# Performance work log

Measured on AMD Instinct MI355X. Metric: run time of the kernel, lower is better.

## Reference

```python
import jax, jax.numpy as jnp
import numpy as np

N_USERS = 1024
N_ITEMS = 2048
N = N_USERS + N_ITEMS          # 3072 total nodes
D = 128                        # latent_dim_rec
L = 3                          # n_layers
K = [64, 64, 64]               # top-k per layer for getMaskAdj
GAMMA = 0.2                    # residual weight on svd embeddings
X_SCALE = 1.0                  # delta
B = 8192                       # batch of (user, item) pairs


def setup_inputs() -> dict:
    key = jax.random.key(0)
    ks = jax.random.split(key, 9)
    # normalized-adjacency-like dense graph: nonnegative, row sums ~ 1
    A = jax.random.uniform(ks[0], (N, N), dtype=jnp.float32) * (2.0 / N)
    user_emb = jax.random.normal(ks[1], (N_USERS, D), dtype=jnp.float32)
    item_emb = jax.random.normal(ks[2], (N_ITEMS, D), dtype=jnp.float32)
    user_emb0 = jax.random.normal(ks[3], (N_USERS, D), dtype=jnp.float32)
    item_emb0 = jax.random.normal(ks[4], (N_ITEMS, D), dtype=jnp.float32)
    vector_u = jax.random.uniform(ks[5], (1, N), dtype=jnp.float32)
    vector_v = jax.random.uniform(ks[6], (1, N), dtype=jnp.float32)
    users = jax.random.randint(ks[7], (B,), 0, N_USERS)
    items = jax.random.randint(ks[8], (B,), 0, N_ITEMS)
    return {
        "users": users, "items": items, "A": A,
        "user_emb": user_emb, "item_emb": item_emb,
        "user_emb0": user_emb0, "item_emb0": item_emb0,
        "vector_u": vector_u, "vector_v": vector_v,
    }


def topk_mask(M, k):
    """Keep top-k entries per row of M, zero elsewhere (getMaskAdj)."""
    vals, idx = jax.lax.top_k(M, k)          # [N,k], [N,k]
    rows = jnp.arange(M.shape[0])[:, None]
    return jnp.zeros_like(M).at[rows, idx].set(vals)


def _computer(A, user_emb, item_emb, user_emb0, item_emb0, vector_u, vector_v):
    all_emb = jnp.concatenate([user_emb, item_emb], axis=0)      # [N,D]
    all_emb0 = jnp.concatenate([user_emb0, item_emb0], axis=0)   # [N,D]
    u = vector_u[0]  # [N]
    v = vector_v[0]  # [N]

    # ---- computAttention: w_k = u A^k v for k = 0..L (A^0 = I via A_0=eye) ----
    w_list = [jnp.dot(u, v)]
    powers = []           # A^1 .. A^L (g_droped progression)
    Ak = A
    for layer in range(L):
        powers.append(Ak)
        w_list.append(jnp.dot(u, Ak @ v))
        if layer < L - 1:
            Ak = A @ Ak   # g_droped = Graph @ A_k
    w = jnp.stack(w_list)                 # [L+1]
    w = w / jnp.sum(w)
    attention_weight = jax.nn.softmax(w)  # softmax(dim=0)

    # ---- getMaskAdj: top-k masked powers ----
    A_list = [topk_mask(powers[l], K[l]) if K[l] != 0 else powers[l] for l in range(L)]

    # ---- layer-wise propagation with attention-weighted accumulation ----
    emb0 = all_emb
    light_out = X_SCALE * attention_weight[0] * all_emb
    for layer in range(L):
        e = A_list[layer] @ emb0 + GAMMA * all_emb0   # SpMM + residual
        light_out = light_out + X_SCALE * attention_weight[layer + 1] * e
    users_all = light_out[:N_USERS]
    items_all = light_out[N_USERS:]
    return users_all, items_all


def reference(users, items, A, user_emb, item_emb, user_emb0, item_emb0, vector_u, vector_v):
    users_all, items_all = _computer(A, user_emb, item_emb, user_emb0, item_emb0, vector_u, vector_v)
    u_e = users_all[users]   # [B,D]
    i_e = items_all[items]   # [B,D]
    return jnp.sum(u_e * i_e, axis=1)  # [B]
```

## Files before the change

kernel.cpp:

```cpp
#include <hip/hip_runtime.h>
#include <hip/hip_fp8.h>
#include <math.h>

#define NN 3072
#define NU 1024
#define NI 2048
#define DD 128
#define BB 8192
#define GAMMA_F 0.2f

#define SCALE_A 524288.0f
#define F8SCALE2 1.9073486328125e-06f
#define DESCALE38 3.637978807091713e-12f

#define KBLK ((size_t)NN * 64)

typedef __attribute__((ext_vector_type(4))) float f32x4;
typedef __attribute__((ext_vector_type(16))) float f32x16;
typedef __attribute__((ext_vector_type(4))) int i32x4;
typedef __attribute__((ext_vector_type(8))) int i32x8;

static __device__ inline unsigned short bf16bits(float x) {
  union { unsigned u; float f; } cv;
  cv.f = x;
  unsigned r = cv.u + 0x7fff + ((cv.u >> 16) & 1);
  return (unsigned short)(r >> 16);
}

static __device__ inline unsigned pk4_f8(float a, float b, float c, float d) {
#if defined(__has_builtin)
#if __has_builtin(__builtin_amdgcn_cvt_pk_fp8_f32)
  int p = __builtin_amdgcn_cvt_pk_fp8_f32(a, b, 0, false);
  p = __builtin_amdgcn_cvt_pk_fp8_f32(c, d, p, true);
  return (unsigned)p;
#else
  return (unsigned)__hip_fp8_e4m3(a).__x | ((unsigned)__hip_fp8_e4m3(b).__x << 8) |
         ((unsigned)__hip_fp8_e4m3(c).__x << 16) |
         ((unsigned)__hip_fp8_e4m3(d).__x << 24);
#endif
#else
  return (unsigned)__hip_fp8_e4m3(a).__x | ((unsigned)__hip_fp8_e4m3(b).__x << 8) |
         ((unsigned)__hip_fp8_e4m3(c).__x << 16) |
         ((unsigned)__hip_fp8_e4m3(d).__x << 24);
#endif
}

static __device__ inline void atomAddF(float* p, float v) {
#if defined(__has_builtin)
#if __has_builtin(__builtin_amdgcn_global_atomic_fadd_f32)
  __builtin_amdgcn_global_atomic_fadd_f32(
      (__attribute__((address_space(1))) float*)p, v);
#else
  unsafeAtomicAdd(p, v);
#endif
#else
  unsafeAtomicAdd(p, v);
#endif
}

static __device__ inline float block_sum(float s, float* red4) {
  int tid = threadIdx.x;
  for (int off = 32; off; off >>= 1) s += __shfl_down(s, off, 64);
  if ((tid & 63) == 0) red4[tid >> 6] = s;
  __syncthreads();
  return red4[0] + red4[1] + red4[2] + red4[3];
}

static __device__ inline float row_dot_f32(const float* __restrict__ a,
                                           const float* __restrict__ b,
                                           float* red4) {
  const float4* ap = (const float4*)a;
  const float4* bp = (const float4*)b;
  float s = 0.f;
  for (int j = threadIdx.x; j < NN / 4; j += 256) {
    float4 x = ap[j], y = bp[j];
    s += x.x * y.x + x.y * y.y + x.z * y.z + x.w * y.w;
  }
  return block_sum(s, red4);
}

static __device__ inline void load48_bf(const unsigned short* __restrict__ b0,
                                        int parts, int row, int lane,
                                        float* f) {
  const uint4* r0 = (const uint4*)(b0 + (size_t)row * NN);
#pragma unroll
  for (int j = 0; j < 6; ++j) {
    uint4 q = r0[lane + j * 64];
    unsigned uu[4] = {q.x, q.y, q.z, q.w};
#pragma unroll
    for (int e = 0; e < 4; ++e) {
      f[j * 8 + e * 2] = __uint_as_float(uu[e] << 16);
      f[j * 8 + e * 2 + 1] = __uint_as_float(uu[e] & 0xffff0000u);
    }
  }
  for (int p = 1; p < parts; ++p) {
    const uint4* rp = (const uint4*)(b0 + (size_t)p * NN * NN + (size_t)row * NN);
#pragma unroll
    for (int j = 0; j < 6; ++j) {
      uint4 q = rp[lane + j * 64];
      unsigned uu[4] = {q.x, q.y, q.z, q.w};
#pragma unroll
      for (int e = 0; e < 4; ++e) {
        f[j * 8 + e * 2] += __uint_as_float(uu[e] << 16);
        f[j * 8 + e * 2 + 1] += __uint_as_float(uu[e] & 0xffff0000u);
      }
    }
  }
}

static __device__ inline void load48_f32(const float* __restrict__ A, int row,
                                         int lane, float* f) {
  const float4* r0 = (const float4*)(A + (size_t)row * NN);
#pragma unroll
  for (int j = 0; j < 12; ++j) {
    float4 a = r0[lane + j * 64];
    f[j * 4 + 0] = a.x; f[j * 4 + 1] = a.y;
    f[j * 4 + 2] = a.z; f[j * 4 + 3] = a.w;
  }
}

static __device__ void select_compact(const float* f, int lane, float descale,
                                      int bf, int* __restrict__ outCnt,
                                      int* __restrict__ outIdx,
                                      float* __restrict__ outVal) {
  unsigned bor = 0, band = 0xffffffffu;
#pragma unroll
  for (int r = 0; r < 48; ++r) {
    unsigned k = __float_as_uint(f[r]);
    bor |= k; band &= k;
  }
  for (int off = 32; off; off >>= 1) {
    bor |= (unsigned)__shfl_xor((int)bor, off, 64);
    band &= (unsigned)__shfl_xor((int)band, off, 64);
  }
  unsigned diff = bor ^ band;
  int hi = diff ? (31 - __clz(diff)) : 16;
  if (hi < 16) hi = 16;
  if (hi > 30) hi = 30;
  unsigned t = band & ~((2u << hi) - 1u);

  int b = hi;
  while (b >= 17) {
    unsigned base = 1u << (b - 1);
    unsigned cand1 = t | base;
    unsigned cand2 = t | (base << 1);
    unsigned cand3 = cand2 | base;
    int c1 = 0, c2 = 0, c3 = 0;
#pragma unroll
    for (int r = 0; r < 48; ++r) {
      unsigned k = __float_as_uint(f[r]);
      c1 += (k >= cand1) ? 1 : 0;
      c2 += (k >= cand2) ? 1 : 0;
      c3 += (k >= cand3) ? 1 : 0;
    }
    for (int off = 32; off; off >>= 1) {
      c1 += __shfl_xor(c1, off, 64);
      c2 += __shfl_xor(c2, off, 64);
      c3 += __shfl_xor(c3, off, 64);
    }
    if (c3 >= 64) t = cand3;
    else if (c2 >= 64) t = cand2;
    else if (c1 >= 64) t = cand1;
    b -= 2;
  }
  if (b == 16) {
    unsigned cand = t | (1u << 16);
    int c = 0;
#pragma unroll
    for (int r = 0; r < 48; ++r) c += (__float_as_uint(f[r]) >= cand) ? 1 : 0;
    for (int off = 32; off; off >>= 1) c += __shfl_xor(c, off, 64);
    if (c >= 64) t = cand;
  }

  int basec = 0;
#pragma unroll
  for (int r = 0; r < 48; ++r) {
    bool keep = __float_as_uint(f[r]) >= t;
    unsigned long long m = __ballot(keep);
    if (keep) {
      int pos = basec + __popcll(m & ((1ull << lane) - 1ull));
      if (pos < 128) {
        int col = bf ? ((r >> 3) * 512 + lane * 8 + (r & 7))
                     : ((r >> 2) * 256 + lane * 4 + (r & 3));
        outIdx[pos] = col << 7;
        outVal[pos] = f[r] * descale;
      }
    }
    basec += __popcll(m);
  }
  if (lane == 0) *outCnt = basec < 128 ? basec : 128;
}

__global__ __launch_bounds__(256) void prep(
    const float* __restrict__ A, const float* __restrict__ vu,
    const float* __restrict__ vv, unsigned char* __restrict__ Af8,
    unsigned char* __restrict__ Atf8, float* __restrict__ y1,
    float* __restrict__ s1) {
  __shared__ float sh[64 * 65 + 512];
  const int bid = blockIdx.x;
  const int t = threadIdx.x;
  const int bx = (bid % 48) * 64, by = (bid / 48) * 64;
  const int rr = t >> 4;
  const int c4 = (t & 15) * 4;
  for (int it = 0; it < 4; ++it) {
    int r = rr + it * 16;
    float4 val = *(const float4*)(A + (size_t)(by + r) * NN + bx + c4);
    sh[r * 65 + c4] = val.x; sh[r * 65 + c4 + 1] = val.y;
    sh[r * 65 + c4 + 2] = val.z; sh[r * 65 + c4 + 3] = val.w;
  }
  __syncthreads();
  {
    int row = t >> 2, ch = t & 3;
    const float* sp = &sh[row * 65 + ch * 16];
    uint4 w;
    w.x = pk4_f8(sp[0] * SCALE_A, sp[1] * SCALE_A, sp[2] * SCALE_A,
                 sp[3] * SCALE_A);
    w.y = pk4_f8(sp[4] * SCALE_A, sp[5] * SCALE_A, sp[6] * SCALE_A,
                 sp[7] * SCALE_A);
    w.z = pk4_f8(sp[8] * SCALE_A, sp[9] * SCALE_A, sp[10] * SCALE_A,
                 sp[11] * SCALE_A);
    w.w = pk4_f8(sp[12] * SCALE_A, sp[13] * SCALE_A, sp[14] * SCALE_A,
                 sp[15] * SCALE_A);
    *(uint4*)(Af8 + (size_t)(bx >> 6) * KBLK + (size_t)(by + row) * 64 +
              ch * 16) = w;
  }
  {
    int c = t >> 2, ch = t & 3;
    float v[16];
#pragma unroll
    for (int e = 0; e < 16; ++e) v[e] = sh[(ch * 16 + e) * 65 + c];
    uint4 w;
    w.x = pk4_f8(v[0] * SCALE_A, v[1] * SCALE_A, v[2] * SCALE_A,
                 v[3] * SCALE_A);
    w.y = pk4_f8(v[4] * SCALE_A, v[5] * SCALE_A, v[6] * SCALE_A,
                 v[7] * SCALE_A);
    w.z = pk4_f8(v[8] * SCALE_A, v[9] * SCALE_A, v[10] * SCALE_A,
                 v[11] * SCALE_A);
    w.w = pk4_f8(v[12] * SCALE_A, v[13] * SCALE_A, v[14] * SCALE_A,
                 v[15] * SCALE_A);
    *(uint4*)(Atf8 + (size_t)(by >> 6) * KBLK + (size_t)(bx + c) * 64 +
              ch * 16) = w;
  }
  const int q = t >> 6;
  const int l = t & 63;
  float sy = 0.f, ss_ = 0.f;
  for (int i = 0; i < 16; ++i) {
    int c = q * 16 + i;
    sy += sh[l * 65 + c] * vv[bx + c];
    ss_ += vu[by + c] * sh[c * 65 + l];
  }
  float* red = sh + 64 * 65;
  red[q * 64 + l] = sy;
  red[256 + q * 64 + l] = ss_;
  __syncthreads();
  if (t < 64) {
    float v4 = red[t] + red[64 + t] + red[128 + t] + red[192 + t];
    atomAddF(&y1[by + t], v4);
  } else if (t < 128) {
    int cc = t - 64;
    float v4 = red[256 + cc] + red[256 + 64 + cc] + red[256 + 128 + cc] +
               red[256 + 192 + cc];
    atomAddF(&s1[bx + cc], v4);
  }
}

#define MFMA4(A0, A1, B0, B1)                                          \
  acc[0][0] = __builtin_amdgcn_mfma_scale_f32_32x32x64_f8f6f4(         \
      A0, B0, acc[0][0], 0, 0, 0, 127, 0, 127);                        \
  acc[0][1] = __builtin_amdgcn_mfma_scale_f32_32x32x64_f8f6f4(         \
      A0, B1, acc[0][1], 0, 0, 0, 127, 0, 127);                        \
  acc[1][0] = __builtin_amdgcn_mfma_scale_f32_32x32x64_f8f6f4(         \
      A1, B0, acc[1][0], 0, 0, 0, 127, 0, 127);                        \
  acc[1][1] = __builtin_amdgcn_mfma_scale_f32_32x32x64_f8f6f4(         \
      A1, B1, acc[1][1], 0, 0, 0, 127, 0, 127);

static __device__ inline i32x8 ldfragL(const char* p) {
  i32x4 lo = *(const i32x4*)p;
  i32x4 hi = *(const i32x4*)(p + 1024);
  return (i32x8){lo.x, lo.y, lo.z, lo.w, hi.x, hi.y, hi.z, hi.w};
}

__global__ __launch_bounds__(256) void gemm_f8(
    const unsigned char* __restrict__ Ag,
    const unsigned char* __restrict__ Btg,
    unsigned short* __restrict__ Cg) {
  __shared__ char smem[2][16384];
  const int wg = blockIdx.x;
  const int xcd = wg & 7;
  const int idx = wg >> 3;
  const int bxi = xcd * 3 + (idx % 3);
  const int byi = idx / 3;
  const int rowBase = byi * 128, colBase = bxi * 128;

  const int t = threadIdx.x;
  const int w = t >> 6, l = t & 63;
  const int wr = w >> 1, wc = w & 1;
  const int r32 = l & 31, hh = l >> 5;

  f32x16 acc[2][2];
  for (int i = 0; i < 2; ++i)
    for (int j = 0; j < 2; ++j)
      for (int e = 0; e < 16; ++e) acc[i][j][e] = 0.f;

  const unsigned char* aT = Ag + (size_t)rowBase * 64;
  const unsigned char* bT = Btg + (size_t)colBase * 64;
  const int laneOff = r32 * 64 + hh * 32;

#define STAGE(kt, b)                                                        \
  {                                                                         \
    const size_t kOff = (size_t)(kt) * KBLK;                                \
    _Pragma("unroll") for (int r_ = 0; r_ < 4; ++r_) {                      \
      int q_ = r_ * 4 + w;                                                  \
      int s_ = (q_ >> 1) & 3, h_ = q_ & 1;                                  \
      const unsigned char* g_ = ((q_ < 8) ? aT : bT) + kOff +               \
                                (size_t)(s_ * 32) * 64 + laneOff + h_ * 16; \
      __builtin_amdgcn_global_load_lds(                                     \
          (const __attribute__((address_space(1))) unsigned*)g_,            \
          (__attribute__((address_space(3))) unsigned*)(smem[b] +           \
                                                        q_ * 1024),         \
          16, 0, 0);                                                        \
    }                                                                       \
  }

  const int nt = NN / 64;
  STAGE(0, 0);
  __syncthreads();
  int cur = 0;
  for (int kt = 0; kt < nt; ++kt) {
    if (kt + 1 < nt) STAGE(kt + 1, cur ^ 1);
    const char* sb = smem[cur];
    i32x8 a0 = ldfragL(sb + (wr * 2 + 0) * 2048 + l * 16);
    i32x8 a1 = ldfragL(sb + (wr * 2 + 1) * 2048 + l * 16);
    i32x8 b0 = ldfragL(sb + 8192 + (wc * 2 + 0) * 2048 + l * 16);
    i32x8 b1 = ldfragL(sb + 8192 + (wc * 2 + 1) * 2048 + l * 16);
    MFMA4(a0, a1, b0, b1);
    __syncthreads();
    cur ^= 1;
  }
#undef STAGE

  for (int i = 0; i < 2; ++i) {
    int rb = rowBase + wr * 64 + i * 32 + 4 * hh;
    for (int j = 0; j < 2; ++j) {
      int cc = colBase + wc * 64 + j * 32 + r32;
      for (int reg = 0; reg < 16; ++reg) {
        int rr = rb + (reg & 3) + 8 * (reg >> 2);
        Cg[(size_t)rr * NN + cc] = bf16bits(acc[i][j][reg]);
      }
    }
  }
}

__global__ __launch_bounds__(256) void post1(
    const unsigned short* __restrict__ C, int parts,
    const float* __restrict__ A, const float* __restrict__ y1,
    unsigned char* __restrict__ A2f8, int* __restrict__ cnts1,
    int* __restrict__ tIdx1, float* __restrict__ tVal1,
    float* __restrict__ tvec, const float* __restrict__ uemb,
    const float* __restrict__ iemb, float* __restrict__ allE) {
  const int bid = blockIdx.x;
  const int t = threadIdx.x;
  if (bid < 768) {
    int row = bid * 4 + (t >> 6);
    int lane = t & 63;
    float f[48];
    load48_bf(C, parts, row, lane, f);
#pragma unroll
    for (int j = 0; j < 6; ++j) {
      uint2 w;
      w.x = pk4_f8(f[j * 8 + 0] * F8SCALE2, f[j * 8 + 1] * F8SCALE2,
                   f[j * 8 + 2] * F8SCALE2, f[j * 8 + 3] * F8SCALE2);
      w.y = pk4_f8(f[j * 8 + 4] * F8SCALE2, f[j * 8 + 5] * F8SCALE2,
                   f[j * 8 + 6] * F8SCALE2, f[j * 8 + 7] * F8SCALE2);
      size_t addr = (size_t)(j * 8 + (lane >> 3)) * KBLK +
                    (size_t)row * 64 + (lane & 7) * 8;
      *(uint2*)(A2f8 + addr) = w;
    }
    select_compact(f, lane, DESCALE38, 1, &cnts1[row],
                   tIdx1 + (size_t)row * 128, tVal1 + (size_t)row * 128);
  } else if (bid < 1536) {
    int row = (bid - 768) * 4 + (t >> 6);
    int lane = t & 63;
    const float4* rp = (const float4*)(A + (size_t)row * NN);
    const float4* yp = (const float4*)y1;
    float s = 0.f;
#pragma unroll
    for (int j = 0; j < 12; ++j) {
      float4 a = rp[lane + j * 64];
      float4 y = yp[lane + j * 64];
      s += a.x * y.x + a.y * y.y + a.z * y.z + a.w * y.w;
    }
    for (int off = 32; off; off >>= 1) s += __shfl_down(s, off, 64);
    if (lane == 0) tvec[row] = s;
  } else {
    int idx = (bid - 1536) * 256 + t;
    int e = idx * 4;
    float4 v = (e < NU * DD) ? *(const float4*)(uemb + e)
                             : *(const float4*)(iemb + (e - NU * DD));
    *(float4*)(allE + e) = v;
  }
}

__global__ __launch_bounds__(256) void post2(
    const float* __restrict__ vu, const float* __restrict__ vv,
    const float* __restrict__ y1, const float* __restrict__ s1,
    const float* __restrict__ tvec, float* __restrict__ wacc) {
  __shared__ float red4[4];
  const int t = threadIdx.x;
  float w0 = row_dot_f32(vu, vv, red4);  __syncthreads();
  float w1 = row_dot_f32(vu, y1, red4);  __syncthreads();
  float w2 = row_dot_f32(s1, y1, red4);  __syncthreads();
  float w3 = row_dot_f32(s1, tvec, red4);
  if (t == 0) { wacc[0] = w0; wacc[1] = w1; wacc[2] = w2; wacc[3] = w3; }
}

__global__ __launch_bounds__(256) void sel02(
    const unsigned short* __restrict__ C, int parts,
    const float* __restrict__ A, int* __restrict__ cnt0,
    int* __restrict__ idx0, float* __restrict__ val0,
    int* __restrict__ cnt2, int* __restrict__ idx2,
    float* __restrict__ val2) {
  const int bid = blockIdx.x;
  const int t = threadIdx.x;
  const int w = t >> 6, lane = t & 63;
  const int row = (bid >> 1) * 4 + w;
  float f[48];
  if ((bid & 1) == 0) {
    load48_bf(C, parts, row, lane, f);
    select_compact(f, lane, DESCALE38, 1, &cnt2[row],
                   idx2 + (size_t)row * 128, val2 + (size_t)row * 128);
  } else {
    load48_f32(A, row, lane, f);
    select_compact(f, lane, 1.0f, 0, &cnt0[row],
                   idx0 + (size_t)row * 128, val0 + (size_t)row * 128);
  }
}

__global__ __launch_bounds__(256) void gather_light(
    const float* __restrict__ allE, const float* __restrict__ uemb0,
    const float* __restrict__ iemb0, const float* __restrict__ wacc,
    const int* __restrict__ cnt0, const int* __restrict__ idx0,
    const float* __restrict__ val0, const int* __restrict__ cnts1,
    const int* __restrict__ tIdx1, const float* __restrict__ tVal1,
    const int* __restrict__ cnt2, const int* __restrict__ idx2,
    const float* __restrict__ val2, float* __restrict__ lightOut) {
  __shared__ int li[4][384];
  __shared__ float lv[4][384];
  const int t = threadIdx.x;
  const int w = t >> 6, lane = t & 63;
  const int row = blockIdx.x * 4 + w;

  float w0 = wacc[0], w1 = wacc[1], w2 = wacc[2], w3 = wacc[3];
  float ss = w0 + w1 + w2 + w3;
  w0 /= ss; w1 /= ss; w2 /= ss; w3 /= ss;
  float m = fmaxf(fmaxf(w0, w1), fmaxf(w2, w3));
  float ex0 = expf(w0 - m), ex1 = expf(w1 - m), ex2 = expf(w2 - m),
        ex3 = expf(w3 - m);
  float se = ex0 + ex1 + ex2 + ex3;
  float aw0 = ex0 / se, aw1 = ex1 / se, aw2 = ex2 / se, aw3 = ex3 / se;
  float aw4 = GAMMA_F * (aw1 + aw2 + aw3);

  const int c0 = cnt0[row], c1 = cnts1[row], c2 = cnt2[row];
  const int p0 = (c0 + 7) & ~7, p1 = (c1 + 7) & ~7, p2 = (c2 + 7) & ~7;
  int* Li = li[w];
  float* Lv = lv[w];
  const size_t rb = (size_t)row * 128;
  for (int k = lane; k < p0; k += 64) {
    bool in = k < c0;
    Li[k] = in ? idx0[rb + k] : 0;
    Lv[k] = in ? aw1 * val0[rb + k] : 0.f;
  }
  for (int k = lane; k < p1; k += 64) {
    bool in = k < c1;
    Li[p0 + k] = in ? tIdx1[rb + k] : 0;
    Lv[p0 + k] = in ? aw2 * tVal1[rb + k] : 0.f;
  }
  for (int k = lane; k < p2; k += 64) {
    bool in = k < c2;
    Li[p0 + p1 + k] = in ? idx2[rb + k] : 0;
    Lv[p0 + p1 + k] = in ? aw3 * val2[rb + k] : 0.f;
  }

  const int ct = p0 + p1 + p2;
  const float2* E2 = (const float2*)allE;
  float ax = 0.f, ay = 0.f, bx_ = 0.f, by_ = 0.f;
  for (int k = 0; k < ct; k += 8) {
    int i0 = Li[k + 0], i1 = Li[k + 1], i2 = Li[k + 2], i3 = Li[k + 3];
    int i4 = Li[k + 4], i5 = Li[k + 5], i6 = Li[k + 6], i7 = Li[k + 7];
    float v0 = Lv[k + 0], v1 = Lv[k + 1], v2 = Lv[k + 2], v3 = Lv[k + 3];
    float v4 = Lv[k + 4], v5 = Lv[k + 5], v6 = Lv[k + 6], v7 = Lv[k + 7];
    float2 g0 = E2[(i0 >> 1) + lane];
    float2 g1 = E2[(i1 >> 1) + lane];
    float2 g2 = E2[(i2 >> 1) + lane];
    float2 g3 = E2[(i3 >> 1) + lane];
    float2 g4 = E2[(i4 >> 1) + lane];
    float2 g5 = E2[(i5 >> 1) + lane];
    float2 g6 = E2[(i6 >> 1) + lane];
    float2 g7 = E2[(i7 >> 1) + lane];
    ax += v0 * g0.x; ay += v0 * g0.y;
    bx_ += v1 * g1.x; by_ += v1 * g1.y;
    ax += v2 * g2.x; ay += v2 * g2.y;
    bx_ += v3 * g3.x; by_ += v3 * g3.y;
    ax += v4 * g4.x; ay += v4 * g4.y;
    bx_ += v5 * g5.x; by_ += v5 * g5.y;
    ax += v6 * g6.x; ay += v6 * g6.y;
    bx_ += v7 * g7.x; by_ += v7 * g7.y;
  }
  float2 sE = E2[((size_t)row << 6) + lane];
  float2 e0 = (row < NU)
                  ? ((const float2*)uemb0)[(size_t)row * 64 + lane]
                  : ((const float2*)iemb0)[(size_t)(row - NU) * 64 + lane];
  float ox = (ax + bx_) + aw0 * sE.x + aw4 * e0.x;
  float oy = (ay + by_) + aw0 * sE.y + aw4 * e0.y;
  float2 o; o.x = ox; o.y = oy;
  ((float2*)lightOut)[(size_t)row * 64 + lane] = o;
}

__global__ __launch_bounds__(256) void out_dot(const int* __restrict__ users,
                                               const int* __restrict__ items,
                                               const float* __restrict__ lightOut,
                                               float* __restrict__ out) {
  int b = blockIdx.x * 4 + (threadIdx.x >> 6);
  int lane = threadIdx.x & 63;
  const float* up = lightOut + (size_t)users[b] * DD;
  const float* ip = lightOut + (size_t)(NU + items[b]) * DD;
  float s = up[lane] * ip[lane] + up[lane + 64] * ip[lane + 64];
  for (int off = 32; off; off >>= 1) s += __shfl_down(s, off, 64);
  if (lane == 0) out[b] = s;
}

extern "C" void kernel_launch(void* const* d_in, const int* in_sizes, int n_in,
                              void* d_out, int out_size, void* d_ws,
                              size_t ws_size, hipStream_t stream) {
  const int* users = (const int*)d_in[0];
  const int* items = (const int*)d_in[1];
  const float* A = (const float*)d_in[2];
  const float* uemb = (const float*)d_in[3];
  const float* iemb = (const float*)d_in[4];
  const float* uemb0 = (const float*)d_in[5];
  const float* iemb0 = (const float*)d_in[6];
  const float* vu = (const float*)d_in[7];
  const float* vv = (const float*)d_in[8];
  float* out = (float*)d_out;

  char* ws = (char*)d_ws;
  size_t off = 0;
  auto alloc = [&](size_t bytes) -> void* {
    void* p = ws + off;
    off += (bytes + 255) & ~(size_t)255;
    return p;
  };
  unsigned char* Af8 = (unsigned char*)alloc((size_t)NN * NN);
  unsigned char* Atf8 = (unsigned char*)alloc((size_t)NN * NN);
  unsigned char* A2f8 = (unsigned char*)alloc((size_t)NN * NN);
  float* y1 = (float*)alloc((size_t)NN * 4);
  float* s1 = (float*)alloc((size_t)NN * 4);
  float* tvec = (float*)alloc((size_t)NN * 4);
  float* wacc = (float*)alloc(256);
  int* cnts1 = (int*)alloc((size_t)NN * 4);
  int* tIdx1 = (int*)alloc((size_t)NN * 128 * 4);
  float* tVal1 = (float*)alloc((size_t)NN * 128 * 4);
  float* lightOut = (float*)alloc((size_t)NN * DD * 4);
  int* cnt0 = (int*)alloc((size_t)NN * 4);
  int* cnt2 = (int*)alloc((size_t)NN * 4);

  float* allE = (float*)Af8;
  const size_t LSTB = (size_t)NN * 128 * 4;
  int* idx0 = (int*)(Atf8);
  float* val0 = (float*)(Atf8 + LSTB);
  int* idx2 = (int*)(Atf8 + 2 * LSTB);
  float* val2 = (float*)(Atf8 + 3 * LSTB);

  unsigned short* C = (unsigned short*)alloc((size_t)NN * NN * 2);

  hipMemsetAsync(y1, 0, (size_t)2 * NN * 4, stream);
  prep<<<2304, 256, 0, stream>>>(A, vu, vv, Af8, Atf8, y1, s1);
  gemm_f8<<<576, 256, 0, stream>>>(Af8, Atf8, C);
  post1<<<1920, 256, 0, stream>>>(C, 1, A, y1, A2f8, cnts1, tIdx1,
                                  tVal1, tvec, uemb, iemb, allE);
  gemm_f8<<<576, 256, 0, stream>>>(A2f8, Atf8, C);
  sel02<<<1536, 256, 0, stream>>>(C, 1, A, cnt0, idx0, val0, cnt2, idx2,
                                  val2);
  post2<<<1, 256, 0, stream>>>(vu, vv, y1, s1, tvec, wacc);
  gather_light<<<768, 256, 0, stream>>>(allE, uemb0, iemb0, wacc, cnt0, idx0,
                                        val0, cnts1, tIdx1, tVal1, cnt2, idx2,
                                        val2, lightOut);
  out_dot<<<BB / 4, 256, 0, stream>>>(users, items, lightOut, out);
}
```

Baseline: 263.9 us.

## Triple-buffer FP8 GEMM pipeline and fold small kernels into neighbors

The FP8 GEMM moves from a double-buffered LDS pipeline to a triple-buffered one. It prefetches two K-tiles ahead, waits on explicit vmcnt instead of full syncthreads, and raises wave priority around the MFMAs. The embedding concat copy moves from post1 into extra prep blocks, writing to a dedicated allE buffer instead of aliasing Af8. The single-block attention-weight reduction kernel is merged into sel02 as one extra block, which removes a launch. The triple buffer uses more LDS per block, and the relaxed barrier protocol relies on the vmcnt counts being correct.

```diff
diff --git a/kernel.cpp b/kernel.cpp
--- a/kernel.cpp
+++ b/kernel.cpp
@@ -195,10 +195,19 @@
     const float* __restrict__ A, const float* __restrict__ vu,
     const float* __restrict__ vv, unsigned char* __restrict__ Af8,
     unsigned char* __restrict__ Atf8, float* __restrict__ y1,
-    float* __restrict__ s1) {
+    float* __restrict__ s1, const float* __restrict__ uemb,
+    const float* __restrict__ iemb, float* __restrict__ allE) {
   __shared__ float sh[64 * 65 + 512];
   const int bid = blockIdx.x;
   const int t = threadIdx.x;
+  if (bid >= 2304) {
+    int idx = (bid - 2304) * 256 + t;
+    int e = idx * 4;
+    float4 v = (e < NU * DD) ? *(const float4*)(uemb + e)
+                             : *(const float4*)(iemb + (e - NU * DD));
+    *(float4*)(allE + e) = v;
+    return;
+  }
   const int bx = (bid % 48) * 64, by = (bid / 48) * 64;
   const int rr = t >> 4;
   const int c4 = (t & 15) * 4;
@@ -284,7 +293,7 @@
     const unsigned char* __restrict__ Ag,
     const unsigned char* __restrict__ Btg,
     unsigned short* __restrict__ Cg) {
-  __shared__ char smem[2][16384];
+  __shared__ char smem[3][16384];
   const int wg = blockIdx.x;
   const int xcd = wg & 7;
   const int idx = wg >> 3;
@@ -324,18 +333,25 @@
 
   const int nt = NN / 64;
   STAGE(0, 0);
-  __syncthreads();
-  int cur = 0;
+  STAGE(1, 1);
   for (int kt = 0; kt < nt; ++kt) {
-    if (kt + 1 < nt) STAGE(kt + 1, cur ^ 1);
-    const char* sb = smem[cur];
+    if (kt < nt - 1) {
+      asm volatile("s_waitcnt vmcnt(4)" ::: "memory");
+    } else {
+      asm volatile("s_waitcnt vmcnt(0)" ::: "memory");
+    }
+    __builtin_amdgcn_s_barrier();
+    __builtin_amdgcn_sched_barrier(0);
+    const char* sb = smem[kt % 3];
     i32x8 a0 = ldfragL(sb + (wr * 2 + 0) * 2048 + l * 16);
     i32x8 a1 = ldfragL(sb + (wr * 2 + 1) * 2048 + l * 16);
     i32x8 b0 = ldfragL(sb + 8192 + (wc * 2 + 0) * 2048 + l * 16);
     i32x8 b1 = ldfragL(sb + 8192 + (wc * 2 + 1) * 2048 + l * 16);
+    if (kt + 2 < nt) STAGE(kt + 2, (kt + 2) % 3);
+    __builtin_amdgcn_s_setprio(1);
     MFMA4(a0, a1, b0, b1);
-    __syncthreads();
-    cur ^= 1;
+    __builtin_amdgcn_s_setprio(0);
+    __builtin_amdgcn_sched_barrier(0);
   }
 #undef STAGE
 
@@ -356,8 +372,7 @@
     const float* __restrict__ A, const float* __restrict__ y1,
     unsigned char* __restrict__ A2f8, int* __restrict__ cnts1,
     int* __restrict__ tIdx1, float* __restrict__ tVal1,
-    float* __restrict__ tvec, const float* __restrict__ uemb,
-    const float* __restrict__ iemb, float* __restrict__ allE) {
+    float* __restrict__ tvec) {
   const int bid = blockIdx.x;
   const int t = threadIdx.x;
   if (bid < 768) {
@@ -378,7 +393,7 @@
     }
     select_compact(f, lane, DESCALE38, 1, &cnts1[row],
                    tIdx1 + (size_t)row * 128, tVal1 + (size_t)row * 128);
-  } else if (bid < 1536) {
+  } else {
     int row = (bid - 768) * 4 + (t >> 6);
     int lane = t & 63;
     const float4* rp = (const float4*)(A + (size_t)row * NN);
@@ -392,26 +407,7 @@
     }
     for (int off = 32; off; off >>= 1) s += __shfl_down(s, off, 64);
     if (lane == 0) tvec[row] = s;
-  } else {
-    int idx = (bid - 1536) * 256 + t;
-    int e = idx * 4;
-    float4 v = (e < NU * DD) ? *(const float4*)(uemb + e)
-                             : *(const float4*)(iemb + (e - NU * DD));
-    *(float4*)(allE + e) = v;
-  }
-}
-
-__global__ __launch_bounds__(256) void post2(
-    const float* __restrict__ vu, const float* __restrict__ vv,
-    const float* __restrict__ y1, const float* __restrict__ s1,
-    const float* __restrict__ tvec, float* __restrict__ wacc) {
-  __shared__ float red4[4];
-  const int t = threadIdx.x;
-  float w0 = row_dot_f32(vu, vv, red4);  __syncthreads();
-  float w1 = row_dot_f32(vu, y1, red4);  __syncthreads();
-  float w2 = row_dot_f32(s1, y1, red4);  __syncthreads();
-  float w3 = row_dot_f32(s1, tvec, red4);
-  if (t == 0) { wacc[0] = w0; wacc[1] = w1; wacc[2] = w2; wacc[3] = w3; }
+  }
 }
 
 __global__ __launch_bounds__(256) void sel02(
@@ -419,9 +415,21 @@
     const float* __restrict__ A, int* __restrict__ cnt0,
     int* __restrict__ idx0, float* __restrict__ val0,
     int* __restrict__ cnt2, int* __restrict__ idx2,
-    float* __restrict__ val2) {
+    float* __restrict__ val2, const float* __restrict__ vu,
+    const float* __restrict__ vv, const float* __restrict__ y1,
+    const float* __restrict__ s1, const float* __restrict__ tvec,
+    float* __restrict__ wacc) {
+  __shared__ float red4[4];
   const int bid = blockIdx.x;
   const int t = threadIdx.x;
+  if (bid == 1536) {
+    float w0 = row_dot_f32(vu, vv, red4);  __syncthreads();
+    float w1 = row_dot_f32(vu, y1, red4);  __syncthreads();
+    float w2 = row_dot_f32(s1, y1, red4);  __syncthreads();
+    float w3 = row_dot_f32(s1, tvec, red4);
+    if (t == 0) { wacc[0] = w0; wacc[1] = w1; wacc[2] = w2; wacc[3] = w3; }
+    return;
+  }
   const int w = t >> 6, lane = t & 63;
   const int row = (bid >> 1) * 4 + w;
   float f[48];
@@ -563,8 +571,8 @@
   float* lightOut = (float*)alloc((size_t)NN * DD * 4);
   int* cnt0 = (int*)alloc((size_t)NN * 4);
   int* cnt2 = (int*)alloc((size_t)NN * 4);
-
-  float* allE = (float*)Af8;
+  float* allE = (float*)alloc((size_t)NN * DD * 4);
+
   const size_t LSTB = (size_t)NN * 128 * 4;
   int* idx0 = (int*)(Atf8);
   float* val0 = (float*)(Atf8 + LSTB);
@@ -574,14 +582,14 @@
   unsigned short* C = (unsigned short*)alloc((size_t)NN * NN * 2);
 
   hipMemsetAsync(y1, 0, (size_t)2 * NN * 4, stream);
-  prep<<<2304, 256, 0, stream>>>(A, vu, vv, Af8, Atf8, y1, s1);
+  prep<<<2688, 256, 0, stream>>>(A, vu, vv, Af8, Atf8, y1, s1, uemb, iemb,
+                                 allE);
   gemm_f8<<<576, 256, 0, stream>>>(Af8, Atf8, C);
-  post1<<<1920, 256, 0, stream>>>(C, 1, A, y1, A2f8, cnts1, tIdx1,
-                                  tVal1, tvec, uemb, iemb, allE);
+  post1<<<1536, 256, 0, stream>>>(C, 1, A, y1, A2f8, cnts1, tIdx1, tVal1,
+                                  tvec);
   gemm_f8<<<576, 256, 0, stream>>>(A2f8, Atf8, C);
-  sel02<<<1536, 256, 0, stream>>>(C, 1, A, cnt0, idx0, val0, cnt2, idx2,
-                                  val2);
-  post2<<<1, 256, 0, stream>>>(vu, vv, y1, s1, tvec, wacc);
+  sel02<<<1537, 256, 0, stream>>>(C, 1, A, cnt0, idx0, val0, cnt2, idx2,
+                                  val2, vu, vv, y1, s1, tvec, wacc);
   gather_light<<<768, 256, 0, stream>>>(allE, uemb0, iemb0, wacc, cnt0, idx0,
                                         val0, cnts1, tIdx1, tVal1, cnt2, idx2,
                                         val2, lightOut);
```

After: 259.0 us. Within noise of the previous version (-1.8%).
